# Optimization experiments

Hardware: AMD Instinct MI355X
Metric: run time of the kernel (lower is better)

## Reference

```python
import jax, jax.numpy as jnp
import numpy as np


def setup_inputs() -> dict:
    key = jax.random.key(0)
    k1, k2 = jax.random.split(key)
    B, C_in, C_out, H, W = 16, 64, 64, 256, 256
    MH, MW = 8, 12
    x = jax.random.normal(k1, (B, C_in, H, W), dtype=jnp.float32)
    scale = 1.0 / np.sqrt(C_in * C_out).astype(np.float32)
    weight = scale * jax.random.normal(k2, (C_in, C_out, MH, MW, 2), dtype=jnp.float32)
    return {"x": x, "weight": weight}


def reference(x, weight):
    B, C, H, W = x.shape
    Wr = W // 2 + 1  # rfft width
    mh = min(weight.shape[2], H)
    mw = min(weight.shape[3], Wr)
    # FFT to frequency domain (orthonormal), keep only low-frequency block
    x_ft = jnp.fft.rfft2(x, norm='ortho')  # (B, C_in, H, Wr) complex
    w_cplx = (weight[..., 0] + 1j * weight[..., 1])[:, :, :mh, :mw]  # (C_in, C_out, mh, mw)
    out_modes = jnp.einsum('bixy,ioxy->boxy', x_ft[:, :, :mh, :mw], w_cplx)
    out_ft = jnp.zeros((B, weight.shape[1], H, Wr), dtype=out_modes.dtype)
    out_ft = out_ft.at[:, :, :mh, :mw].set(out_modes)
    return jnp.fft.irfft2(out_ft, s=(H, W), norm='ortho')
```

## Files before the change

kernel.cpp:

```cpp
#include <hip/hip_runtime.h>
#include <math.h>

#define PI2 6.2831853071795864769f


__global__ __launch_bounds__(256) void k1_fwd(const float* __restrict__ x,
                                              float* __restrict__ Xm) {
  __shared__ float tw[128][16];
  __shared__ float lds[2][4096];
  const int img  = blockIdx.x;
  const int wv   = threadIdx.x >> 6;
  const int lane = threadIdx.x & 63;

  {
    int h = threadIdx.x >> 1;
    int kyb = (threadIdx.x & 1) * 4;
#pragma unroll
    for (int j = 0; j < 4; ++j) {
      int ky = kyb + j;
      float th = PI2 * (float)((ky * h) & 255) * (1.0f / 256.0f);
      float s_, c_;
      __sincosf(th, &s_, &c_);
      tw[h][ky * 2] = c_;
      tw[h][ky * 2 + 1] = -s_;
    }
  }
  __syncthreads();

  float aR[8][4], aI[8][4];
#pragma unroll
  for (int ky = 0; ky < 8; ++ky)
#pragma unroll
    for (int j = 0; j < 4; ++j) { aR[ky][j] = 0.0f; aI[ky][j] = 0.0f; }

  const float* xa = x + (size_t)img * 65536 + (size_t)(wv * 32) * 256 + lane * 4;
  const float* xb = xa + 128 * 256;
  for (int it = 0; it < 32; ++it) {
    const int h = wv * 32 + it;
    float4 va = *(const float4*)xa;
    float4 vb = *(const float4*)xb;
    xa += 256; xb += 256;
    float p0 = va.x + vb.x, p1 = va.y + vb.y, p2 = va.z + vb.z, p3 = va.w + vb.w;
    float m0 = va.x - vb.x, m1 = va.y - vb.y, m2 = va.z - vb.z, m3 = va.w - vb.w;
#pragma unroll
    for (int ky = 0; ky < 8; ++ky) {
      float c  = tw[h][ky * 2];
      float ns = tw[h][ky * 2 + 1];
      float u0, u1, u2, u3;
      if (ky & 1) { u0 = m0; u1 = m1; u2 = m2; u3 = m3; }
      else        { u0 = p0; u1 = p1; u2 = p2; u3 = p3; }
      aR[ky][0] = fmaf(u0, c, aR[ky][0]);  aI[ky][0] = fmaf(u0, ns, aI[ky][0]);
      aR[ky][1] = fmaf(u1, c, aR[ky][1]);  aI[ky][1] = fmaf(u1, ns, aI[ky][1]);
      aR[ky][2] = fmaf(u2, c, aR[ky][2]);  aI[ky][2] = fmaf(u2, ns, aI[ky][2]);
      aR[ky][3] = fmaf(u3, c, aR[ky][3]);  aI[ky][3] = fmaf(u3, ns, aI[ky][3]);
    }
  }

  if (wv < 2) {
#pragma unroll
    for (int ky = 0; ky < 8; ++ky)
#pragma unroll
      for (int j = 0; j < 4; ++j) {
        int p = (ky * 256 + lane * 4 + j) * 2;
        lds[wv][p] = aR[ky][j];
        lds[wv][p + 1] = aI[ky][j];
      }
  }
  __syncthreads();
  if (wv >= 2) {
#pragma unroll
    for (int ky = 0; ky < 8; ++ky)
#pragma unroll
      for (int j = 0; j < 4; ++j) {
        int p = (ky * 256 + lane * 4 + j) * 2;
        lds[wv - 2][p] += aR[ky][j];
        lds[wv - 2][p + 1] += aI[ky][j];
      }
  }
  __syncthreads();
  for (int f = threadIdx.x; f < 4096; f += 256) lds[0][f] += lds[1][f];
  __syncthreads();

  if (threadIdx.x < 96) {
    int ky = threadIdx.x / 12, kx = threadIdx.x % 12;
    float Cw, Sw;
    __sincosf(PI2 * (float)kx * (1.0f / 256.0f), &Sw, &Cw);
    float c = 1.0f, s = 0.0f, Xr = 0.0f, Xi = 0.0f;
    const float* base = &lds[0][ky * 512];
    for (int w = 0; w < 256; ++w) {
      float Sre = base[w * 2], Sim = base[w * 2 + 1];
      Xr += Sre * c + Sim * s;
      Xi += Sim * c - Sre * s;
      float nc = fmaf(c, Cw, -s * Sw);
      s = fmaf(s, Cw, c * Sw);
      c = nc;
    }
    float2 v = { Xr * (1.0f / 256.0f), Xi * (1.0f / 256.0f) };
    const int bb = img >> 6, ii = img & 63;
    ((float2*)Xm)[(size_t)(bb * 96 + threadIdx.x) * 64 + ii] = v;
  }
}

__global__ __launch_bounds__(256) void k2_fused(const float* __restrict__ Xm,
                                                const float* __restrict__ wt,
                                                float* __restrict__ outp) {
  __shared__ float sh[6528];
  __shared__ float Fs[192];
  const int img2 = blockIdx.x;
  const int b = img2 >> 6, o = img2 & 63;
  const int tid = threadIdx.x;

  float fr = 0.0f, fi = 0.0f;
#pragma unroll
  for (int c = 0; c < 2; ++c) {
    for (int idx = tid; idx < 1536; idx += 256) {
      int p = idx >> 4, j4 = idx & 15;
      float4 v = ((const float4*)(Xm + (size_t)(b * 96 + p) * 128 + c * 64))[j4];
      ((float4*)(sh + p * 68))[j4] = v;
    }
    __syncthreads();
    if (tid < 96) {
      const int pos = tid;
      const float* wrow = wt + ((size_t)(c * 2048 + o) * 96 + pos) * 2;
#pragma unroll 8
      for (int jj = 0; jj < 32; ++jj) {
        float xr = sh[pos * 68 + 2 * jj];
        float xi = sh[pos * 68 + 2 * jj + 1];
        float wr = wrow[(size_t)jj * 12288];
        float wi = wrow[(size_t)jj * 12288 + 1];
        fr += xr * wr - xi * wi;
        fi += xr * wi + xi * wr;
      }
    }
    __syncthreads();
  }
  if (tid < 96) { Fs[tid * 2] = fr; Fs[tid * 2 + 1] = fi; }
  __syncthreads();

  {
    const int h = tid;
    float cc[8], ss[8];
#pragma unroll
    for (int ky = 0; ky < 8; ++ky) {
      float th = PI2 * (float)((ky * h) & 255) * (1.0f / 256.0f);
      __sincosf(th, &ss[ky], &cc[ky]);
    }
    float4 ov4[6];
    float* ov = (float*)ov4;
#pragma unroll
    for (int kx = 0; kx < 12; ++kx) {
      float Ur = 0.0f, Ui = 0.0f;
#pragma unroll
      for (int ky = 0; ky < 8; ++ky) {
        float Fr = Fs[(ky * 12 + kx) * 2], Fi = Fs[(ky * 12 + kx) * 2 + 1];
        Ur += Fr * cc[ky] - Fi * ss[ky];
        Ui += Fr * ss[ky] + Fi * cc[ky];
      }
      float a = (kx == 0 ? 1.0f : 2.0f) * (1.0f / 256.0f);
      ov[kx * 2] = Ur * a;
      ov[kx * 2 + 1] = Ui * a;
    }
    float4* dst = (float4*)(sh + h * 24);
#pragma unroll
    for (int k = 0; k < 6; ++k) dst[k] = ov4[k];
  }
  __syncthreads();

  {
    const int wv = tid >> 6, lane = tid & 63;
    float cx[12], sx[12];
#pragma unroll
    for (int kx = 0; kx < 12; ++kx) {
      float th = PI2 * (float)((kx * lane) & 255) * (1.0f / 256.0f);
      __sincosf(th, &sx[kx], &cx[kx]);
    }
    float* ob = outp + (size_t)img2 * 65536 + lane;
    for (int l0 = 0; l0 < 64; ++l0) {
      const int h = wv * 64 + l0;
      const float4* ur = (const float4*)(sh + h * 24);
      float u[24];
#pragma unroll
      for (int k = 0; k < 6; ++k) {
        float4 q = ur[k];
        u[4 * k] = q.x; u[4 * k + 1] = q.y; u[4 * k + 2] = q.z; u[4 * k + 3] = q.w;
      }
      float A[4] = {0.0f, 0.0f, 0.0f, 0.0f};
      float B1 = 0.0f, B3 = 0.0f;
#pragma unroll
      for (int kx = 0; kx < 12; ++kx) {
        const int cls = kx & 3;
        A[cls] = fmaf(u[2 * kx], cx[kx], A[cls]);
        A[cls] = fmaf(-u[2 * kx + 1], sx[kx], A[cls]);
        if (cls == 1) {
          B1 = fmaf(u[2 * kx], sx[kx], B1);
          B1 = fmaf(u[2 * kx + 1], cx[kx], B1);
        }
        if (cls == 3) {
          B3 = fmaf(u[2 * kx], sx[kx], B3);
          B3 = fmaf(u[2 * kx + 1], cx[kx], B3);
        }
      }
      float t0 = A[0] + A[2], t1 = A[1] + A[3];
      float t2 = A[0] - A[2], t3 = B3 - B1;
      float* row = ob + h * 256;
      row[0]   = t0 + t1;
      row[64]  = t2 + t3;
      row[128] = t0 - t1;
      row[192] = t2 - t3;
    }
  }
}

extern "C" void kernel_launch(void* const* d_in, const int* in_sizes, int n_in,
                              void* d_out, int out_size, void* d_ws, size_t ws_size,
                              hipStream_t stream) {
  const float* x  = (const float*)d_in[0];
  const float* wt = (const float*)d_in[1];
  float* outp = (float*)d_out;

  float* Xm = (float*)d_ws;

  k1_fwd  <<<1024, 256, 0, stream>>>(x, Xm);
  k2_fused<<<1024, 256, 0, stream>>>(Xm, wt, outp);
}
```

Baseline: 477.4 us.

## Split serial DFT and channel contraction across two thread halves, padded LDS layout

The forward kernel swaps the per-row twiddle table for a single 256-entry cos/sin table indexed incrementally. It pads the partial-sum LDS layout with a stride of 17 to avoid bank conflicts and folds the cross-wave reduction into the final W-direction DFT. That DFT and the channel contraction in the second kernel now run on 192 threads, each half handling part of the range, with an extra LDS reduction step. This cuts the serial critical path that used only 96 threads, at the cost of extra syncs and some scratch LDS; launch bounds also add a min-blocks hint.

Result: no change. 471.1 us (-1.3%).

```diff
diff --git a/kernel.cpp b/kernel.cpp
--- a/kernel.cpp
+++ b/kernel.cpp
@@ -4,26 +4,19 @@
 #define PI2 6.2831853071795864769f
 
 
-__global__ __launch_bounds__(256) void k1_fwd(const float* __restrict__ x,
-                                              float* __restrict__ Xm) {
-  __shared__ float tw[128][16];
-  __shared__ float lds[2][4096];
+__global__ __launch_bounds__(256, 4) void k1_fwd(const float* __restrict__ x,
+                                                 float* __restrict__ Xm) {
+  __shared__ float2 ctab[256];
+  __shared__ float lds[2][4352];
+  __shared__ float scr[192];
   const int img  = blockIdx.x;
   const int wv   = threadIdx.x >> 6;
   const int lane = threadIdx.x & 63;
 
   {
-    int h = threadIdx.x >> 1;
-    int kyb = (threadIdx.x & 1) * 4;
-#pragma unroll
-    for (int j = 0; j < 4; ++j) {
-      int ky = kyb + j;
-      float th = PI2 * (float)((ky * h) & 255) * (1.0f / 256.0f);
-      float s_, c_;
-      __sincosf(th, &s_, &c_);
-      tw[h][ky * 2] = c_;
-      tw[h][ky * 2 + 1] = -s_;
-    }
+    float s_, c_;
+    __sincosf(PI2 * (float)threadIdx.x * (1.0f / 256.0f), &s_, &c_);
+    ctab[threadIdx.x] = make_float2(c_, s_);
   }
   __syncthreads();
 
@@ -35,8 +28,11 @@
 
   const float* xa = x + (size_t)img * 65536 + (size_t)(wv * 32) * 256 + lane * 4;
   const float* xb = xa + 128 * 256;
+  int idx[8];
+#pragma unroll
+  for (int ky = 0; ky < 8; ++ky) idx[ky] = (ky * (wv * 32)) & 255;
+
   for (int it = 0; it < 32; ++it) {
-    const int h = wv * 32 + it;
     float4 va = *(const float4*)xa;
     float4 vb = *(const float4*)xb;
     xa += 256; xb += 256;
@@ -44,8 +40,10 @@
     float m0 = va.x - vb.x, m1 = va.y - vb.y, m2 = va.z - vb.z, m3 = va.w - vb.w;
 #pragma unroll
     for (int ky = 0; ky < 8; ++ky) {
-      float c  = tw[h][ky * 2];
-      float ns = tw[h][ky * 2 + 1];
+      float2 cs = ctab[idx[ky]];
+      float c  = cs.x;
+      float ns = -cs.y;
+      idx[ky] = (idx[ky] + ky) & 255;
       float u0, u1, u2, u3;
       if (ky & 1) { u0 = m0; u1 = m1; u2 = m2; u3 = m3; }
       else        { u0 = p0; u1 = p1; u2 = p2; u3 = p3; }
@@ -61,8 +59,8 @@
     for (int ky = 0; ky < 8; ++ky)
 #pragma unroll
       for (int j = 0; j < 4; ++j) {
-        int p = (ky * 256 + lane * 4 + j) * 2;
-        lds[wv][p] = aR[ky][j];
+        int p = (lane * 4 + j) * 17 + ky * 2;
+        lds[wv][p]     = aR[ky][j];
         lds[wv][p + 1] = aI[ky][j];
       }
   }
@@ -72,31 +70,44 @@
     for (int ky = 0; ky < 8; ++ky)
 #pragma unroll
       for (int j = 0; j < 4; ++j) {
-        int p = (ky * 256 + lane * 4 + j) * 2;
-        lds[wv - 2][p] += aR[ky][j];
+        int p = (lane * 4 + j) * 17 + ky * 2;
+        lds[wv - 2][p]     += aR[ky][j];
         lds[wv - 2][p + 1] += aI[ky][j];
       }
   }
   __syncthreads();
-  for (int f = threadIdx.x; f < 4096; f += 256) lds[0][f] += lds[1][f];
-  __syncthreads();
-
-  if (threadIdx.x < 96) {
-    int ky = threadIdx.x / 12, kx = threadIdx.x % 12;
+
+  float Xr = 0.0f, Xi = 0.0f;
+  if (threadIdx.x < 192) {
+    const int pos  = threadIdx.x % 96;
+    const int half = threadIdx.x / 96;
+    const int ky = pos / 12, kx = pos % 12;
     float Cw, Sw;
     __sincosf(PI2 * (float)kx * (1.0f / 256.0f), &Sw, &Cw);
-    float c = 1.0f, s = 0.0f, Xr = 0.0f, Xi = 0.0f;
-    const float* base = &lds[0][ky * 512];
-    for (int w = 0; w < 256; ++w) {
-      float Sre = base[w * 2], Sim = base[w * 2 + 1];
+    float c = ((kx & 1) && half) ? -1.0f : 1.0f;
+    float s = 0.0f;
+    const float* b0 = &lds[0][(half * 128) * 17 + ky * 2];
+    const float* b1 = &lds[1][(half * 128) * 17 + ky * 2];
+    for (int w = 0; w < 128; ++w) {
+      float Sre = b0[w * 17]     + b1[w * 17];
+      float Sim = b0[w * 17 + 1] + b1[w * 17 + 1];
       Xr += Sre * c + Sim * s;
       Xi += Sim * c - Sre * s;
       float nc = fmaf(c, Cw, -s * Sw);
       s = fmaf(s, Cw, c * Sw);
       c = nc;
     }
-    float2 v = { Xr * (1.0f / 256.0f), Xi * (1.0f / 256.0f) };
+    if (threadIdx.x >= 96) {
+      scr[(threadIdx.x - 96) * 2]     = Xr;
+      scr[(threadIdx.x - 96) * 2 + 1] = Xi;
+    }
+  }
+  __syncthreads();
+  if (threadIdx.x < 96) {
+    float xr = (Xr + scr[threadIdx.x * 2])     * (1.0f / 256.0f);
+    float xi = (Xi + scr[threadIdx.x * 2 + 1]) * (1.0f / 256.0f);
     const int bb = img >> 6, ii = img & 63;
+    float2 v = { xr, xi };
     ((float2*)Xm)[(size_t)(bb * 96 + threadIdx.x) * 64 + ii] = v;
   }
 }
@@ -111,6 +122,8 @@
   const int tid = threadIdx.x;
 
   float fr = 0.0f, fi = 0.0f;
+  const int mpos = tid % 96;
+  const int mh2  = tid / 96;
 #pragma unroll
   for (int c = 0; c < 2; ++c) {
     for (int idx = tid; idx < 1536; idx += 256) {
@@ -119,13 +132,14 @@
       ((float4*)(sh + p * 68))[j4] = v;
     }
     __syncthreads();
-    if (tid < 96) {
-      const int pos = tid;
-      const float* wrow = wt + ((size_t)(c * 2048 + o) * 96 + pos) * 2;
-#pragma unroll 8
-      for (int jj = 0; jj < 32; ++jj) {
-        float xr = sh[pos * 68 + 2 * jj];
-        float xi = sh[pos * 68 + 2 * jj + 1];
+    if (tid < 192) {
+      const float* wrow =
+          wt + (((size_t)(c * 32 + mh2 * 16) * 64 + o) * 96 + mpos) * 2;
+      const float* xrow = sh + mpos * 68 + mh2 * 32;
+#pragma unroll
+      for (int jj = 0; jj < 16; ++jj) {
+        float xr = xrow[2 * jj];
+        float xi = xrow[2 * jj + 1];
         float wr = wrow[(size_t)jj * 12288];
         float wi = wrow[(size_t)jj * 12288 + 1];
         fr += xr * wr - xi * wi;
@@ -134,7 +148,15 @@
     }
     __syncthreads();
   }
-  if (tid < 96) { Fs[tid * 2] = fr; Fs[tid * 2 + 1] = fi; }
+  if (tid >= 96 && tid < 192) {
+    Fs[(tid - 96) * 2]     = fr;
+    Fs[(tid - 96) * 2 + 1] = fi;
+  }
+  __syncthreads();
+  if (tid < 96) {
+    Fs[tid * 2]     += fr;
+    Fs[tid * 2 + 1] += fi;
+  }
   __syncthreads();
 
   {
```
